# Optimization experiments

Hardware: AMD Instinct MI355X
Metric: run time of the kernel (lower is better)

The kernel has to match this reference:

```python
import jax, jax.numpy as jnp
import numpy as np

EPS = 1e-3  # tfa GroupNormalization default epsilon
H = 8       # num heads


def group_norm(x, gamma, beta):
    # x: [..., E]; per-sample group norm over each group of head_dim channels
    lead, E = x.shape[:-1], x.shape[-1]
    D = E // H
    xg = x.reshape(lead + (H, D))
    mu = xg.mean(-1, keepdims=True)
    var = xg.var(-1, keepdims=True)
    xg = (xg - mu) * jax.lax.rsqrt(var + EPS)
    xg = xg * gamma.reshape(H, D) + beta.reshape(H, D)
    return xg.reshape(lead + (E,))


def in_proj(x, W, b, gamma, beta):
    # Dense -> CELU(alpha=1) == ELU -> GroupNorm(groups=H)
    return group_norm(jax.nn.elu(x @ W + b), gamma, beta)


def setup_inputs() -> dict:
    B, M, E, MID = 16, 2048, 1024, 64
    D = E // H
    ks = jax.random.split(jax.random.key(0), 16)
    w = lambda k, shape: jax.random.normal(k, shape, jnp.float32) * 0.02
    inp = {
        "query": jax.random.normal(ks[0], (B, E), jnp.float32),
        "key": jax.random.normal(ks[1], (B * M, E), jnp.float32),
        "mask": jnp.ones((B, M), jnp.float32),
        "value1": jax.random.normal(ks[2], (B, E), jnp.float32),
        "value2": jax.random.normal(ks[3], (B * M, E), jnp.float32),
        # four in-projection layers: Dense(E,E) + GroupNorm gamma/beta
        "Wq": w(ks[4], (E, E)), "bq": jnp.zeros((E,), jnp.float32), "gq": jnp.ones((E,), jnp.float32), "Bq": jnp.zeros((E,), jnp.float32),
        "Wk": w(ks[5], (E, E)), "bk": jnp.zeros((E,), jnp.float32), "gk": jnp.ones((E,), jnp.float32), "Bk": jnp.zeros((E,), jnp.float32),
        "Wv1": w(ks[6], (E, E)), "bv1": jnp.zeros((E,), jnp.float32), "gv1": jnp.ones((E,), jnp.float32), "Bv1": jnp.zeros((E,), jnp.float32),
        "Wv2": w(ks[7], (E, E)), "bv2": jnp.zeros((E,), jnp.float32), "gv2": jnp.ones((E,), jnp.float32), "Bv2": jnp.zeros((E,), jnp.float32),
        # XLASCAtt: basic Dense(head_dim->64)+ReLU; last Dense(64->1); last2 Dense(64->head_dim)
        "Wb": w(ks[8], (D, MID)), "bb": jnp.zeros((MID,), jnp.float32),
        "Wl1": w(ks[9], (MID, 1)), "bl1": jnp.zeros((1,), jnp.float32),
        "Wl2": w(ks[10], (MID, D)), "bl2": jnp.zeros((D,), jnp.float32),
    }
    return inp


def reference(query, key, mask, value1, value2,
              Wq, bq, gq, Bq, Wk, bk, gk, Bk,
              Wv1, bv1, gv1, Bv1, Wv2, bv2, gv2, Bv2,
              Wb, bb, Wl1, bl1, Wl2, bl2):
    B, E = query.shape
    D = E // H
    # in-projections
    q = in_proj(query, Wq, bq, gq, Bq).reshape(B, H, D)            # [B,H,D]
    v1 = in_proj(value1, Wv1, bv1, gv1, Bv1).reshape(B, H, D)      # [B,H,D]
    k = in_proj(key, Wk, bk, gk, Bk).reshape(B, -1, H, D).transpose(0, 2, 1, 3)       # [B,H,M,D]
    v2 = in_proj(value2, Wv2, bv2, gv2, Bv2).reshape(B, -1, H, D).transpose(0, 2, 1, 3)  # [B,H,M,D]

    # low-rank bilinear attention map: elementwise q*k per head
    att_map = q[:, :, None, :] * k                                 # [B,H,M,D]
    basic = jax.nn.relu(att_map @ Wb + bb)                         # [B,H,M,MID]

    # masked mean-pool over memory positions
    m_ext = mask[:, None, :, None]                                 # [B,1,M,1]
    pool = (basic * m_ext).sum(-2) / m_ext.sum(-2)                 # [B,H,MID]

    # spatial attention (softmax over M) and channel gate (sigmoid)
    alpha_sp = (basic @ Wl1 + bl1)[..., 0]                         # [B,H,M]
    alpha_sp = jnp.where(mask[:, None, :] == 0, -1e9, alpha_sp)
    alpha_sp = jax.nn.softmax(alpha_sp, axis=-1)
    alpha_ch = jax.nn.sigmoid(pool @ Wl2 + bl2)                    # [B,H,D]

    v2_agg = jnp.einsum('bhm,bhmd->bhd', alpha_sp, v2)             # [B,H,D]
    attn = v1 * v2_agg * alpha_ch                                  # [B,H,D]
    return attn.reshape(B, H * D)
```

## Files before the change

### kernel.cpp

```cpp
#include <hip/hip_runtime.h>
#include <hip/hip_bf16.h>
#include <math.h>

typedef __attribute__((ext_vector_type(8))) short bf16x8;
typedef __attribute__((ext_vector_type(4))) float f32x4;
typedef __attribute__((ext_vector_type(8))) unsigned short u16x8;

typedef const float* fptr;
typedef const unsigned short* bfp;

__device__ inline float b2f(unsigned short u) {
    union { unsigned int i; float f; } v; v.i = ((unsigned int)u) << 16; return v.f;
}
__device__ inline unsigned short f2b(float x) {
    __hip_bfloat16 h = __float2bfloat16(x);
    return *(unsigned short*)&h;
}
__device__ inline float elu_f(float x) { return x > 0.f ? x : __expf(x) - 1.f; }

__device__ inline void load_lds16(const void* g, void* l) {
    __builtin_amdgcn_global_load_lds(
        (const __attribute__((address_space(1))) unsigned int*)g,
        (__attribute__((address_space(3))) unsigned int*)l, 16, 0, 0);
}

__global__ __launch_bounds__(256) void prep(
    fptr key, fptr value2, unsigned short* AbfK, unsigned short* AbfV2,
    fptr Wk, fptr Wv2, unsigned short* WtK, unsigned short* WtV2,
    fptr Wb, unsigned short* Wbt,
    fptr query, fptr Wq, fptr bq, fptr gq, fptr Bq,
    fptr value1, fptr Wv1, fptr bv1, fptr gv1, fptr Bv1,
    float* qws, float* v1ws)
{
    __shared__ __align__(16) char smem[16640];
    int blk = blockIdx.x, t = threadIdx.x;

    if (blk < 32768) {
        fptr A = (blk < 16384) ? key : value2;
        unsigned short* B = (blk < 16384) ? AbfK : AbfV2;
        size_t idx = ((size_t)(blk & 16383) * 256 + t) * 8;
        const float4* ap = (const float4*)(A + idx);
        float4 a0 = ap[0], a1 = ap[1];
        u16x8 p = { f2b(a0.x), f2b(a0.y), f2b(a0.z), f2b(a0.w),
                    f2b(a1.x), f2b(a1.y), f2b(a1.z), f2b(a1.w) };
        *(u16x8*)(B + idx) = p;
        return;
    }
    if (blk < 33280) {
        float (*tl)[65] = (float (*)[65])smem;
        int idx = blk - 32768;
        fptr W = (idx >> 8) ? Wv2 : Wk;
        unsigned short* Wt = (idx >> 8) ? WtV2 : WtK;
        int k0 = ((idx >> 4) & 15) * 64, n0 = (idx & 15) * 64;
        #pragma unroll
        for (int i = 0; i < 16; i++) {
            int kl = i * 4 + (t >> 6), nl = t & 63;
            tl[kl][nl] = W[(size_t)(k0 + kl) * 1024 + n0 + nl];
        }
        __syncthreads();
        #pragma unroll
        for (int i = 0; i < 16; i++) {
            int nl = i * 4 + (t >> 6), kl = t & 63;
            Wt[(size_t)(n0 + nl) * 1024 + k0 + kl] = f2b(tl[kl][nl]);
        }
        return;
    }
    if (blk == 33280) {
        unsigned short* tb = (unsigned short*)smem;
        for (int i = 0; i < 32; i++) {
            int idx = i * 256 + t;
            tb[(idx & 63) * 128 + (idx >> 6)] = f2b(Wb[idx]);
        }
        __syncthreads();
        for (int i = 0; i < 4; i++) {
            int o = (i * 256 + t) * 8;
            *(u16x8*)&Wbt[o] = *(const u16x8*)&tb[o];
        }
        return;
    }
    {
        float* xs = (float*)smem;
        float (*part)[128] = (float (*)[128])(smem + 4096);
        float (*r4)[2] = (float (*)[2])(smem + 4096 + 1024);
        int idx = blk - 33281;
        int hgrp = idx & 7;
        int row  = (idx >> 3) & 15;
        int which = idx >> 7;
        fptr x  = which ? value1 : query;
        fptr W  = which ? Wv1 : Wq;
        fptr bi = which ? bv1 : bq;
        fptr g  = which ? gv1 : gq;
        fptr be = which ? Bv1 : Bq;
        float* outp = which ? v1ws : qws;
        int lane = t & 63, wv = t >> 6;
        for (int i = t; i < 1024; i += 256) xs[i] = x[row * 1024 + i];
        __syncthreads();
        int cl = t & 127, kh = t >> 7;
        int col = hgrp * 128 + cl;
        float acc = 0.f;
        const float* wp = W + (size_t)(kh * 512) * 1024 + col;
        for (int k = 0; k < 512; k++) acc += xs[kh * 512 + k] * wp[(size_t)k * 1024];
        part[kh][cl] = acc;
        __syncthreads();
        float e = 0.f;
        if (t < 128) e = elu_f(part[0][t] + part[1][t] + bi[col]);
        float s = e, ss = e * e;
        for (int m = 32; m > 0; m >>= 1) { s += __shfl_xor(s, m); ss += __shfl_xor(ss, m); }
        if (lane == 0) { r4[wv][0] = s; r4[wv][1] = ss; }
        __syncthreads();
        float S  = r4[0][0] + r4[1][0] + r4[2][0] + r4[3][0];
        float SS = r4[0][1] + r4[1][1] + r4[2][1] + r4[3][1];
        float mean = S * (1.f / 128.f);
        float var  = SS * (1.f / 128.f) - mean * mean;
        float inv  = rsqrtf(var + 1e-3f);
        if (t < 128) outp[row * 1024 + col] = (e - mean) * inv * g[col] + be[col];
    }
}

__global__ __launch_bounds__(256) void qwb_prep(
    bfp Wbt, const float* qws, unsigned short* qwbuf)
{
    int bh = blockIdx.x;
    int b = bh >> 3, h = bh & 7;
    int t = threadIdx.x;
    #pragma unroll
    for (int i = 0; i < 4; i++) {
        int idx = (i * 256 + t) * 8;
        int d = idx & 127;
        u16x8 wv = *(const u16x8*)&Wbt[idx];
        const float* qp = qws + b * 1024 + h * 128 + d;
        u16x8 o;
        #pragma unroll
        for (int j = 0; j < 8; j++) o[j] = f2b(b2f(wv[j]) * qp[j]);
        *(u16x8*)&qwbuf[(size_t)bh * 8192 + idx] = o;
    }
}

__global__ __launch_bounds__(256, 3) void gemm_fused(
    bfp AK, bfp WtK, fptr bkp, fptr gkp, fptr Bkp,
    bfp AV, bfp WtV, fptr bvp, fptr gvp, fptr Bvp,
    bfp qwb, fptr maskp, fptr bbp, fptr Wl1, fptr bl1,
    float* logits, float* poolpart, __hip_bfloat16* Z)
{
    __shared__ __align__(16) unsigned short pool[17408];
    unsigned short (*As)[128][32] = (unsigned short (*)[128][32])pool;
    unsigned short (*Bs)[128][32] = (unsigned short (*)[128][32])(pool + 8192);
    unsigned short (*Tt)[136]     = (unsigned short (*)[136])pool;
    __shared__ float sstat[128][2][2];
    __shared__ float masksh[128];
    __shared__ float poolred[4][64];

    int which = blockIdx.x >> 8;
    int r0 = (blockIdx.x & 255) * 128;
    int h  = blockIdx.y;
    int n0 = h * 128;
    int b  = r0 >> 11;
    int mloc = r0 & 2047;
    int mt = (r0 >> 7) & 15;
    int t = threadIdx.x, lane = t & 63, w = t >> 6;
    int c = lane & 15, q = lane >> 4;
    int rowbase = (w & 1) * 64, colbase = (w >> 1) * 64;

    bfp A    = which ? AV  : AK;
    bfp Wt   = which ? WtV : WtK;
    fptr bias = which ? bvp : bkp;
    fptr g    = which ? gvp : gkp;
    fptr be   = which ? Bvp : Bkp;

    if (which == 0 && t < 128) masksh[t] = maskp[r0 + t];

    f32x4 acc[4][4];
    const f32x4 fzero = {0.f, 0.f, 0.f, 0.f};
    #pragma unroll
    for (int i = 0; i < 4; i++)
        #pragma unroll
        for (int j = 0; j < 4; j++) acc[i][j] = fzero;

    int srow = lane >> 2;
    int sseg = (lane & 3) * 8;
    const unsigned short* ag = A  + (size_t)(r0 + w * 32 + srow) * 1024 + sseg;
    const unsigned short* bg = Wt + (size_t)(n0 + w * 32 + srow) * 1024 + sseg;

    for (int k0 = 0; k0 < 1024; k0 += 64) {
        load_lds16(ag + k0,                  &As[0][w * 32][0]);
        load_lds16(ag + k0 + 16 * 1024,      &As[0][w * 32 + 16][0]);
        load_lds16(ag + k0 + 32,             &As[1][w * 32][0]);
        load_lds16(ag + k0 + 32 + 16 * 1024, &As[1][w * 32 + 16][0]);
        load_lds16(bg + k0,                  &Bs[0][w * 32][0]);
        load_lds16(bg + k0 + 16 * 1024,      &Bs[0][w * 32 + 16][0]);
        load_lds16(bg + k0 + 32,             &Bs[1][w * 32][0]);
        load_lds16(bg + k0 + 32 + 16 * 1024, &Bs[1][w * 32 + 16][0]);
        __syncthreads();
        #pragma unroll
        for (int p = 0; p < 2; p++) {
            bf16x8 af[4], bfv[4];
            #pragma unroll
            for (int i = 0; i < 4; i++) af[i]  = *(const bf16x8*)&As[p][rowbase + i * 16 + c][q * 8];
            #pragma unroll
            for (int j = 0; j < 4; j++) bfv[j] = *(const bf16x8*)&Bs[p][colbase + j * 16 + c][q * 8];
            #pragma unroll
            for (int i = 0; i < 4; i++)
                #pragma unroll
                for (int j = 0; j < 4; j++)
                    acc[i][j] = __builtin_amdgcn_mfma_f32_16x16x32_bf16(af[i], bfv[j], acc[i][j], 0, 0, 0);
        }
        __syncthreads();
    }

    float bcol[4], gcol[4], Bcol[4];
    #pragma unroll
    for (int j = 0; j < 4; j++) {
        int cg = n0 + colbase + j * 16 + c;
        bcol[j] = bias[cg]; gcol[j] = g[cg]; Bcol[j] = be[cg];
    }
    #pragma unroll
    for (int i = 0; i < 4; i++)
        #pragma unroll
        for (int j = 0; j < 4; j++)
            #pragma unroll
            for (int r = 0; r < 4; r++)
                acc[i][j][r] = elu_f(acc[i][j][r] + bcol[j]);
    #pragma unroll
    for (int i = 0; i < 4; i++) {
        #pragma unroll
        for (int r = 0; r < 4; r++) {
            float s  = acc[i][0][r] + acc[i][1][r] + acc[i][2][r] + acc[i][3][r];
            float ss = acc[i][0][r] * acc[i][0][r] + acc[i][1][r] * acc[i][1][r]
                     + acc[i][2][r] * acc[i][2][r] + acc[i][3][r] * acc[i][3][r];
            for (int m = 1; m < 16; m <<= 1) { s += __shfl_xor(s, m); ss += __shfl_xor(ss, m); }
            if (c == 0) {
                int rl = rowbase + i * 16 + q * 4 + r;
                sstat[rl][w >> 1][0] = s;
                sstat[rl][w >> 1][1] = ss;
            }
        }
    }
    __syncthreads();
    #pragma unroll
    for (int i = 0; i < 4; i++) {
        #pragma unroll
        for (int r = 0; r < 4; r++) {
            int rl = rowbase + i * 16 + q * 4 + r;
            float S  = sstat[rl][0][0] + sstat[rl][1][0];
            float SS = sstat[rl][0][1] + sstat[rl][1][1];
            float mean = S * (1.f / 128.f);
            float var  = SS * (1.f / 128.f) - mean * mean;
            float inv  = rsqrtf(var + 1e-3f);
            #pragma unroll
            for (int j = 0; j < 4; j++) {
                int cl = colbase + j * 16 + c;
                float v = (acc[i][j][r] - mean) * inv * gcol[j] + Bcol[j];
                if (which == 0) Tt[rl][cl] = f2b(v);
                else Z[(size_t)(r0 + rl) * 1024 + n0 + cl] = __float2bfloat16(v);
            }
        }
    }
    if (which != 0) return;
    __syncthreads();

    const unsigned short* qb = qwb + (size_t)(b * 8 + h) * 8192;
    f32x4 acc2[2][4];
    #pragma unroll
    for (int i = 0; i < 2; i++)
        #pragma unroll
        for (int j = 0; j < 4; j++) acc2[i][j] = fzero;
    #pragma unroll
    for (int s = 0; s < 4; s++) {
        bf16x8 af2[2], bfv[4];
        #pragma unroll
        for (int i = 0; i < 2; i++)
            af2[i] = *(const bf16x8*)&Tt[w * 32 + i * 16 + c][s * 32 + q * 8];
        #pragma unroll
        for (int j = 0; j < 4; j++)
            bfv[j] = *(const bf16x8*)&qb[(j * 16 + c) * 128 + s * 32 + q * 8];
        #pragma unroll
        for (int i = 0; i < 2; i++)
            #pragma unroll
            for (int j = 0; j < 4; j++)
                acc2[i][j] = __builtin_amdgcn_mfma_f32_16x16x32_bf16(af2[i], bfv[j], acc2[i][j], 0, 0, 0);
    }

    float bbs[4], wl1s[4];
    #pragma unroll
    for (int j = 0; j < 4; j++) { bbs[j] = bbp[j * 16 + c]; wl1s[j] = Wl1[j * 16 + c]; }
    float bl1v = bl1[0];
    float pp[4] = {0.f, 0.f, 0.f, 0.f};
    #pragma unroll
    for (int i = 0; i < 2; i++) {
        #pragma unroll
        for (int r = 0; r < 4; r++) {
            int ml = w * 32 + i * 16 + q * 4 + r;
            float mv = masksh[ml];
            float lg = 0.f;
            #pragma unroll
            for (int j = 0; j < 4; j++) {
                float basic = fmaxf(acc2[i][j][r] + bbs[j], 0.f);
                lg += basic * wl1s[j];
                pp[j] += basic * mv;
            }
            lg += __shfl_xor(lg, 1); lg += __shfl_xor(lg, 2);
            lg += __shfl_xor(lg, 4); lg += __shfl_xor(lg, 8);
            if (c == 0)
                logits[((size_t)(b * 8 + h)) * 2048 + mloc + ml] = lg + bl1v;
        }
    }
    #pragma unroll
    for (int j = 0; j < 4; j++) {
        pp[j] += __shfl_xor(pp[j], 16);
        pp[j] += __shfl_xor(pp[j], 32);
    }
    if (lane < 16) {
        #pragma unroll
        for (int j = 0; j < 4; j++) poolred[w][j * 16 + c] = pp[j];
    }
    __syncthreads();
    if (t < 64) {
        float p = poolred[0][t] + poolred[1][t] + poolred[2][t] + poolred[3][t];
        poolpart[((size_t)((b * 8 + h) * 16 + mt)) * 64 + t] = p;
    }
}

__global__ __launch_bounds__(512) void finalize_fused(
    const float* logits, const float* poolpart, fptr maskp,
    const __hip_bfloat16* v2buf, const float* v1ws,
    fptr Wl2, fptr bl2, float* out)
{
    __shared__ float alph[2048];
    __shared__ float red[8];
    __shared__ float redm[8];
    __shared__ float pools[64];
    __shared__ float ach[128];
    __shared__ float redl[8][128];
    int h = blockIdx.x, b = blockIdx.y;
    int t = threadIdx.x, lane = t & 63, wv = t >> 6;

    const float* lg = logits + (size_t)(b * 8 + h) * 2048;
    float msum_l = 0.f, mx_l = -1e30f;
    for (int i = t; i < 2048; i += 512) {
        float mv = maskp[b * 2048 + i];
        msum_l += mv;
        float v = (mv == 0.f) ? -1e9f : lg[i];
        alph[i] = v;
        mx_l = fmaxf(mx_l, v);
    }
    for (int mm = 32; mm > 0; mm >>= 1) {
        msum_l += __shfl_xor(msum_l, mm);
        mx_l = fmaxf(mx_l, __shfl_xor(mx_l, mm));
    }
    if (lane == 0) { red[wv] = msum_l; redm[wv] = mx_l; }
    __syncthreads();
    float msum = 0.f, mx = -1e30f;
    #pragma unroll
    for (int i = 0; i < 8; i++) { msum += red[i]; mx = fmaxf(mx, redm[i]); }

    float se = 0.f;
    for (int i = t; i < 2048; i += 512) {
        float e = __expf(alph[i] - mx);
        alph[i] = e;
        se += e;
    }
    for (int mm = 32; mm > 0; mm >>= 1) se += __shfl_xor(se, mm);
    __syncthreads();
    if (lane == 0) red[wv] = se;
    __syncthreads();
    float S = 0.f;
    #pragma unroll
    for (int i = 0; i < 8; i++) S += red[i];
    float invS = 1.f / S;
    for (int i = t; i < 2048; i += 512) alph[i] *= invS;

    if (t < 64) {
        const float* pq = poolpart + ((size_t)(b * 8 + h) * 16) * 64 + t;
        float p = 0.f;
        for (int pt = 0; pt < 16; pt++) p += pq[pt * 64];
        pools[t] = p / msum;
    }
    __syncthreads();
    if (t < 128) {
        float s2 = bl2[t];
        for (int mid = 0; mid < 64; mid++) s2 += pools[mid] * Wl2[mid * 128 + t];
        ach[t] = 1.f / (1.f + __expf(-s2));
    }
    __syncthreads();

    int mo = lane >> 4, d8 = (lane & 15) * 8;
    float acc[8] = {};
    for (int it = 0; it < 64; it++) {
        int m = it * 32 + wv * 4 + mo;
        bf16x8 v8 = *(const bf16x8*)&v2buf[((size_t)(b * 2048 + m)) * 1024 + h * 128 + d8];
        float a = alph[m];
        #pragma unroll
        for (int j = 0; j < 8; j++)
            acc[j] += a * b2f(((unsigned short*)&v8)[j]);
    }
    #pragma unroll
    for (int j = 0; j < 8; j++) {
        acc[j] += __shfl_xor(acc[j], 16);
        acc[j] += __shfl_xor(acc[j], 32);
    }
    if (lane < 16) {
        #pragma unroll
        for (int j = 0; j < 8; j++) redl[wv][d8 + j] = acc[j];
    }
    __syncthreads();
    if (t < 128) {
        float s = 0.f;
        #pragma unroll
        for (int i = 0; i < 8; i++) s += redl[i][t];
        out[b * 1024 + h * 128 + t] = v1ws[b * 1024 + h * 128 + t] * s * ach[t];
    }
}

extern "C" void kernel_launch(void* const* d_in, const int* in_sizes, int n_in,
                              void* d_out, int out_size, void* d_ws, size_t ws_size,
                              hipStream_t stream) {
    fptr query  = (fptr)d_in[0];
    fptr key    = (fptr)d_in[1];
    fptr maskp  = (fptr)d_in[2];
    fptr value1 = (fptr)d_in[3];
    fptr value2 = (fptr)d_in[4];
    fptr Wq = (fptr)d_in[5],  bq = (fptr)d_in[6],  gq = (fptr)d_in[7],  Bq = (fptr)d_in[8];
    fptr Wk = (fptr)d_in[9],  bk = (fptr)d_in[10], gk = (fptr)d_in[11], Bk = (fptr)d_in[12];
    fptr Wv1 = (fptr)d_in[13], bv1 = (fptr)d_in[14], gv1 = (fptr)d_in[15], Bv1 = (fptr)d_in[16];
    fptr Wv2 = (fptr)d_in[17], bv2 = (fptr)d_in[18], gv2 = (fptr)d_in[19], Bv2 = (fptr)d_in[20];
    fptr Wb = (fptr)d_in[21], bb = (fptr)d_in[22];
    fptr Wl1 = (fptr)d_in[23], bl1 = (fptr)d_in[24];
    fptr Wl2 = (fptr)d_in[25], bl2 = (fptr)d_in[26];

    const size_t MB = 1024 * 1024;
    char* w = (char*)d_ws;
    unsigned short* AbfK  = (unsigned short*)w;
    unsigned short* AbfV2 = (unsigned short*)(w + 64 * MB);
    __hip_bfloat16* zV2   = (__hip_bfloat16*)(w + 128 * MB);
    unsigned short* WtK   = (unsigned short*)(w + 192 * MB);
    unsigned short* WtV2  = (unsigned short*)(w + 194 * MB);
    unsigned short* Wbt   = (unsigned short*)(w + 196 * MB);
    unsigned short* qwbuf = (unsigned short*)(w + 196 * MB + 65536);
    float* qws      = (float*)(w + 196 * MB + 65536 + 2 * MB);
    float* v1ws     = qws + 16 * 1024;
    float* logits   = v1ws + 16 * 1024;
    float* poolpart = logits + 16 * 8 * 2048;
    float* out = (float*)d_out;

    hipLaunchKernelGGL(prep, dim3(33537), dim3(256), 0, stream,
                       key, value2, AbfK, AbfV2,
                       Wk, Wv2, WtK, WtV2, Wb, Wbt,
                       query, Wq, bq, gq, Bq, value1, Wv1, bv1, gv1, Bv1,
                       qws, v1ws);
    hipLaunchKernelGGL(qwb_prep, dim3(128), dim3(256), 0, stream,
                       (bfp)Wbt, qws, qwbuf);
    hipLaunchKernelGGL(gemm_fused, dim3(512, 8), dim3(256), 0, stream,
                       (bfp)AbfK, (bfp)WtK, bk, gk, Bk,
                       (bfp)AbfV2, (bfp)WtV2, bv2, gv2, Bv2,
                       (bfp)qwbuf, maskp, bb, Wl1, bl1, logits, poolpart, zV2);
    hipLaunchKernelGGL(finalize_fused, dim3(8, 16), dim3(512), 0, stream,
                       logits, poolpart, maskp, zV2, v1ws, Wl2, bl2, out);
}
```

Before: 596.3 us.

## Fold qwb_prep into gemm_fused, reorder prep blocks, remap grid for XCD L2 locality

Drops the separate qwb_prep kernel. gemm_fused now computes the q-scaled Wb operand on the fly from Wbt and qws, which removes one launch and the qwbuf round trip through memory. The prep kernel's block order is changed so the small q/v1 projection and weight-transpose blocks are scheduled before the large bf16 conversion blocks. The gemm grid is flattened to 1D and remapped so each XCD handles a contiguous range of row tiles across all heads, with the aim of improving L2 reuse of the A tiles. The trade-off is extra per-block conversion ALU work in the second MFMA stage.

```diff
diff --git a/kernel.cpp b/kernel.cpp
--- a/kernel.cpp
+++ b/kernel.cpp
@@ -35,37 +35,7 @@
     __shared__ __align__(16) char smem[16640];
     int blk = blockIdx.x, t = threadIdx.x;
 
-    if (blk < 32768) {
-        fptr A = (blk < 16384) ? key : value2;
-        unsigned short* B = (blk < 16384) ? AbfK : AbfV2;
-        size_t idx = ((size_t)(blk & 16383) * 256 + t) * 8;
-        const float4* ap = (const float4*)(A + idx);
-        float4 a0 = ap[0], a1 = ap[1];
-        u16x8 p = { f2b(a0.x), f2b(a0.y), f2b(a0.z), f2b(a0.w),
-                    f2b(a1.x), f2b(a1.y), f2b(a1.z), f2b(a1.w) };
-        *(u16x8*)(B + idx) = p;
-        return;
-    }
-    if (blk < 33280) {
-        float (*tl)[65] = (float (*)[65])smem;
-        int idx = blk - 32768;
-        fptr W = (idx >> 8) ? Wv2 : Wk;
-        unsigned short* Wt = (idx >> 8) ? WtV2 : WtK;
-        int k0 = ((idx >> 4) & 15) * 64, n0 = (idx & 15) * 64;
-        #pragma unroll
-        for (int i = 0; i < 16; i++) {
-            int kl = i * 4 + (t >> 6), nl = t & 63;
-            tl[kl][nl] = W[(size_t)(k0 + kl) * 1024 + n0 + nl];
-        }
-        __syncthreads();
-        #pragma unroll
-        for (int i = 0; i < 16; i++) {
-            int nl = i * 4 + (t >> 6), kl = t & 63;
-            Wt[(size_t)(n0 + nl) * 1024 + k0 + kl] = f2b(tl[kl][nl]);
-        }
-        return;
-    }
-    if (blk == 33280) {
+    if (blk == 0) {
         unsigned short* tb = (unsigned short*)smem;
         for (int i = 0; i < 32; i++) {
             int idx = i * 256 + t;
@@ -78,11 +48,11 @@
         }
         return;
     }
-    {
+    if (blk < 257) {
         float* xs = (float*)smem;
         float (*part)[128] = (float (*)[128])(smem + 4096);
         float (*r4)[2] = (float (*)[2])(smem + 4096 + 1024);
-        int idx = blk - 33281;
+        int idx = blk - 1;
         int hgrp = idx & 7;
         int row  = (idx >> 3) & 15;
         int which = idx >> 7;
@@ -114,32 +84,44 @@
         float var  = SS * (1.f / 128.f) - mean * mean;
         float inv  = rsqrtf(var + 1e-3f);
         if (t < 128) outp[row * 1024 + col] = (e - mean) * inv * g[col] + be[col];
-    }
-}
-
-__global__ __launch_bounds__(256) void qwb_prep(
-    bfp Wbt, const float* qws, unsigned short* qwbuf)
-{
-    int bh = blockIdx.x;
-    int b = bh >> 3, h = bh & 7;
-    int t = threadIdx.x;
-    #pragma unroll
-    for (int i = 0; i < 4; i++) {
-        int idx = (i * 256 + t) * 8;
-        int d = idx & 127;
-        u16x8 wv = *(const u16x8*)&Wbt[idx];
-        const float* qp = qws + b * 1024 + h * 128 + d;
-        u16x8 o;
-        #pragma unroll
-        for (int j = 0; j < 8; j++) o[j] = f2b(b2f(wv[j]) * qp[j]);
-        *(u16x8*)&qwbuf[(size_t)bh * 8192 + idx] = o;
+        return;
+    }
+    if (blk < 769) {
+        float (*tl)[65] = (float (*)[65])smem;
+        int idx = blk - 257;
+        fptr W = (idx >> 8) ? Wv2 : Wk;
+        unsigned short* Wt = (idx >> 8) ? WtV2 : WtK;
+        int k0 = ((idx >> 4) & 15) * 64, n0 = (idx & 15) * 64;
+        #pragma unroll
+        for (int i = 0; i < 16; i++) {
+            int kl = i * 4 + (t >> 6), nl = t & 63;
+            tl[kl][nl] = W[(size_t)(k0 + kl) * 1024 + n0 + nl];
+        }
+        __syncthreads();
+        #pragma unroll
+        for (int i = 0; i < 16; i++) {
+            int nl = i * 4 + (t >> 6), kl = t & 63;
+            Wt[(size_t)(n0 + nl) * 1024 + k0 + kl] = f2b(tl[kl][nl]);
+        }
+        return;
+    }
+    {
+        int idx = blk - 769;
+        fptr A = (idx < 16384) ? key : value2;
+        unsigned short* B = (idx < 16384) ? AbfK : AbfV2;
+        size_t e = ((size_t)(idx & 16383) * 256 + t) * 8;
+        const float4* ap = (const float4*)(A + e);
+        float4 a0 = ap[0], a1 = ap[1];
+        u16x8 p = { f2b(a0.x), f2b(a0.y), f2b(a0.z), f2b(a0.w),
+                    f2b(a1.x), f2b(a1.y), f2b(a1.z), f2b(a1.w) };
+        *(u16x8*)(B + e) = p;
     }
 }
 
 __global__ __launch_bounds__(256, 3) void gemm_fused(
     bfp AK, bfp WtK, fptr bkp, fptr gkp, fptr Bkp,
     bfp AV, bfp WtV, fptr bvp, fptr gvp, fptr Bvp,
-    bfp qwb, fptr maskp, fptr bbp, fptr Wl1, fptr bl1,
+    bfp Wbt, const float* qws, fptr maskp, fptr bbp, fptr Wl1, fptr bl1,
     float* logits, float* poolpart, __hip_bfloat16* Z)
 {
     __shared__ __align__(16) unsigned short pool[17408];
@@ -150,13 +132,19 @@
     __shared__ float masksh[128];
     __shared__ float poolred[4][64];
 
-    int which = blockIdx.x >> 8;
-    int r0 = (blockIdx.x & 255) * 128;
-    int h  = blockIdx.y;
+    int bid = blockIdx.x;
+    int xcd = bid & 7;
+    int seq = bid >> 3;
+    int grp = seq >> 3;
+    int h   = seq & 7;
+    int which = grp >> 5;
+    int rowtile = xcd * 32 + (grp & 31);
+
+    int r0 = rowtile * 128;
     int n0 = h * 128;
     int b  = r0 >> 11;
     int mloc = r0 & 2047;
-    int mt = (r0 >> 7) & 15;
+    int mt = rowtile & 15;
     int t = threadIdx.x, lane = t & 63, w = t >> 6;
     int c = lane & 15, q = lane >> 4;
     int rowbase = (w & 1) * 64, colbase = (w >> 1) * 64;
@@ -258,7 +246,7 @@
     if (which != 0) return;
     __syncthreads();
 
-    const unsigned short* qb = qwb + (size_t)(b * 8 + h) * 8192;
+    const float* qrow = qws + b * 1024 + h * 128;
     f32x4 acc2[2][4];
     #pragma unroll
     for (int i = 0; i < 2; i++)
@@ -267,12 +255,21 @@
     #pragma unroll
     for (int s = 0; s < 4; s++) {
         bf16x8 af2[2], bfv[4];
+        float qv[8];
+        #pragma unroll
+        for (int e = 0; e < 8; e++) qv[e] = qrow[s * 32 + q * 8 + e];
         #pragma unroll
         for (int i = 0; i < 2; i++)
             af2[i] = *(const bf16x8*)&Tt[w * 32 + i * 16 + c][s * 32 + q * 8];
         #pragma unroll
-        for (int j = 0; j < 4; j++)
-            bfv[j] = *(const bf16x8*)&qb[(j * 16 + c) * 128 + s * 32 + q * 8];
+        for (int j = 0; j < 4; j++) {
+            bf16x8 wv = *(const bf16x8*)&Wbt[(j * 16 + c) * 128 + s * 32 + q * 8];
+            bf16x8 bv;
+            #pragma unroll
+            for (int e = 0; e < 8; e++)
+                bv[e] = (short)f2b(b2f((unsigned short)wv[e]) * qv[e]);
+            bfv[j] = bv;
+        }
         #pragma unroll
         for (int i = 0; i < 2; i++)
             #pragma unroll
@@ -435,7 +432,6 @@
     unsigned short* WtK   = (unsigned short*)(w + 192 * MB);
     unsigned short* WtV2  = (unsigned short*)(w + 194 * MB);
     unsigned short* Wbt   = (unsigned short*)(w + 196 * MB);
-    unsigned short* qwbuf = (unsigned short*)(w + 196 * MB + 65536);
     float* qws      = (float*)(w + 196 * MB + 65536 + 2 * MB);
     float* v1ws     = qws + 16 * 1024;
     float* logits   = v1ws + 16 * 1024;
@@ -447,12 +443,10 @@
                        Wk, Wv2, WtK, WtV2, Wb, Wbt,
                        query, Wq, bq, gq, Bq, value1, Wv1, bv1, gv1, Bv1,
                        qws, v1ws);
-    hipLaunchKernelGGL(qwb_prep, dim3(128), dim3(256), 0, stream,
-                       (bfp)Wbt, qws, qwbuf);
-    hipLaunchKernelGGL(gemm_fused, dim3(512, 8), dim3(256), 0, stream,
+    hipLaunchKernelGGL(gemm_fused, dim3(4096), dim3(256), 0, stream,
                        (bfp)AbfK, (bfp)WtK, bk, gk, Bk,
                        (bfp)AbfV2, (bfp)WtV2, bv2, gv2, Bv2,
-                       (bfp)qwbuf, maskp, bb, Wl1, bl1, logits, poolpart, zV2);
+                       (bfp)Wbt, qws, maskp, bb, Wl1, bl1, logits, poolpart, zV2);
     hipLaunchKernelGGL(finalize_fused, dim3(8, 16), dim3(512), 0, stream,
                        logits, poolpart, maskp, zV2, v1ws, Wl2, bl2, out);
 }
```

Result: faster. 578.5 us (-3.0%).
